# Performance work log

Measured on AMD Instinct MI355X. Metric: run time of the kernel, lower is better.

## Reference

```python
import jax, jax.numpy as jnp
import numpy as np

IN_F = 4096
OUT_F = 4096
SPARSITY = 0.98
N_TOKENS = 8192


def _structured_mask_and_weight(key):
    # Replicates _initialize_structured_sparsity: each output neuron i gets
    # connections_per_neuron contiguous (mod in_features) input columns
    # starting at (i * cpn) % in_features, with He-style init on those entries.
    num_conn = int((1.0 - SPARSITY) * IN_F * OUT_F)
    cpn = max(1, num_conn // OUT_F)  # connections per neuron (=81 here)
    rows = jnp.arange(OUT_F)[:, None]                      # [out, 1]
    cols = (rows * cpn + jnp.arange(cpn)[None, :]) % IN_F  # [out, cpn]
    mask = jnp.zeros((OUT_F, IN_F), jnp.float32).at[rows, cols].set(1.0)
    vals = jax.random.normal(key, (OUT_F, cpn), jnp.float32) * np.sqrt(2.0 / cpn)
    weight = jnp.zeros((OUT_F, IN_F), jnp.float32).at[rows, cols].set(vals)
    return mask, weight


def setup_inputs() -> dict:
    key = jax.random.key(0)
    k_w, k_b, k_x = jax.random.split(key, 3)
    mask, weight = _structured_mask_and_weight(k_w)
    gauge_field = jnp.ones((OUT_F, IN_F), jnp.float32)  # buffer initialized to ones
    bias = jax.random.normal(k_b, (OUT_F,), jnp.float32) * 0.01
    x = jax.random.normal(k_x, (N_TOKENS, IN_F), jnp.float32)
    return {"x": x, "weight": weight, "bias": bias,
            "mask": mask, "gauge_field": gauge_field}


def reference(x, weight, bias, mask, gauge_field):
    # effective_weight = weight * mask * gauge_field; F.linear(x, W, b) = x @ W.T + b
    effective_weight = weight * mask * gauge_field  # [out, in]
    return jnp.einsum('ni,oi->no', x, effective_weight) + bias
```

## Files before the change

### kernel.cpp

```cpp
#include <hip/hip_runtime.h>


typedef _Float16 h4 __attribute__((ext_vector_type(4)));
typedef _Float16 h8 __attribute__((ext_vector_type(8)));
typedef float f32x4 __attribute__((ext_vector_type(4)));

__global__ void __launch_bounds__(256) build_w4_kernel(
    const float* __restrict__ weight, const float* __restrict__ mask,
    const float* __restrict__ gauge, _Float16* __restrict__ w4) {
  int idx = blockIdx.x * 256 + threadIdx.x;
  int kk = idx % 96;
  int n  = (idx / 96) & 15;
  int m  = idx / 1536;
  int k  = m * 16 + n;
  float v = 0.f;
  if (kk >= n && kk < n + 81) {
    int o   = (2225 * k) & 4095;
    int col = (m * 16 + kk) & 4095;
    size_t off = (size_t)o * 4096 + col;
    v = weight[off] * mask[off] * gauge[off];
  }
  w4[idx] = (_Float16)v;
}

__global__ void __launch_bounds__(1024, 4) spmm_mfma_kernel(
    const float* __restrict__ x, const _Float16* __restrict__ w4,
    const float* __restrict__ bias, float* __restrict__ out) {
  __shared__ __align__(16) _Float16 xl[8 * 4104];
  __shared__ __align__(16) _Float16 ob[8 * 4104];

  const int tid = threadIdx.x;
  const size_t t0 = (size_t)blockIdx.x * 8;

  const float4* xg = (const float4*)(x + t0 * 4096);
#pragma unroll
  for (int i = 0; i < 8; ++i) {
    float4 v = xg[i * 1024 + tid];
    h4 hv = {(_Float16)v.x, (_Float16)v.y, (_Float16)v.z, (_Float16)v.w};
    *(h4*)&xl[i * 4104 + tid * 4] = hv;
  }
  __syncthreads();

  const int w = tid >> 6, lane = tid & 63;
  const int l15 = lane & 15, g = lane >> 4;
  const int tA = l15 & 7;
  const _Float16* xrow = xl + tA * 4104;
  const int aoff = 8 * g;
  const _Float16* bbase = w4 + (size_t)l15 * 96 + 8 * g;

  int m = w * 16;
  const _Float16* bp = bbase + (size_t)m * 1536;
  h8 b0 = *(const h8*)(bp);
  h8 b1 = *(const h8*)(bp + 32);
  h8 b2 = *(const h8*)(bp + 64);

#pragma unroll 2
  for (int i = 0; i < 16; ++i, ++m) {
    const int K16 = m << 4;
    const int o0 = (K16 + aoff) & 4095;
    const int o1 = (K16 + 32 + aoff) & 4095;
    const int o2 = (K16 + 64 + aoff) & 4095;
    h8 a0 = *(const h8*)(xrow + o0);
    h8 a1 = *(const h8*)(xrow + o1);
    h8 a2 = *(const h8*)(xrow + o2);
    h8 nb0, nb1, nb2;
    if (i < 15) {
      const _Float16* np = bbase + (size_t)(m + 1) * 1536;
      nb0 = *(const h8*)(np);
      nb1 = *(const h8*)(np + 32);
      nb2 = *(const h8*)(np + 64);
    } else { nb0 = b0; nb1 = b1; nb2 = b2; }
    f32x4 acc = {0.f, 0.f, 0.f, 0.f};
    acc = __builtin_amdgcn_mfma_f32_16x16x32_f16(a0, b0, acc, 0, 0, 0);
    acc = __builtin_amdgcn_mfma_f32_16x16x32_f16(a1, b1, acc, 0, 0, 0);
    acc = __builtin_amdgcn_mfma_f32_16x16x32_f16(a2, b2, acc, 0, 0, 0);
    if (lane < 32) {
      _Float16* op = ob + (g * 4) * 4104 + K16 + l15;
#pragma unroll
      for (int r = 0; r < 4; ++r) op[r * 4104] = (_Float16)acc[r];
    }
    b0 = nb0; b1 = nb1; b2 = nb2;
  }
  __syncthreads();

  float* og = out + t0 * 4096;
#pragma unroll
  for (int it = 0; it < 32; ++it) {
    int e = it * 1024 + tid;
    int tt = e >> 12, o = e & 4095;
    int k = (81 * o) & 4095;
    og[(size_t)tt * 4096 + o] = (float)ob[tt * 4104 + k] + bias[o];
  }
}

extern "C" void kernel_launch(void* const* d_in, const int* in_sizes, int n_in,
                              void* d_out, int out_size, void* d_ws, size_t ws_size,
                              hipStream_t stream) {
  const float* x      = (const float*)d_in[0];
  const float* weight = (const float*)d_in[1];
  const float* bias   = (const float*)d_in[2];
  const float* mask   = (const float*)d_in[3];
  const float* gauge  = (const float*)d_in[4];
  float* out = (float*)d_out;
  _Float16* w4 = (_Float16*)d_ws;

  build_w4_kernel<<<1536, 256, 0, stream>>>(weight, mask, gauge, w4);
  spmm_mfma_kernel<<<1024, 1024, 0, stream>>>(x, w4, bias, out);
}
```

Before: 358.0 us.

## Reuse x shared buffer for outputs in-place and halve block size

Drops the separate output shared buffer. Results are written back into the x tile in place, trailing the reads by 128 columns, with a barrier on every step and the first chunk held in registers until the end. The row is padded with a wrap-around copy so the masking on the x offsets can go, and blocks shrink to 512 threads, each wave handling 32 chunks. The epilogue writes float4 outputs and loads bias as float4. Halving LDS per block should allow more blocks per CU, at the cost of a __syncthreads in every loop iteration.

Measured after the change: 358.5 us. Within noise of the previous version (+0.2%).

```diff
diff --git a/kernel.cpp b/kernel.cpp
--- a/kernel.cpp
+++ b/kernel.cpp
@@ -4,6 +4,8 @@
 typedef _Float16 h4 __attribute__((ext_vector_type(4)));
 typedef _Float16 h8 __attribute__((ext_vector_type(8)));
 typedef float f32x4 __attribute__((ext_vector_type(4)));
+
+#define XS 4232
 
 __global__ void __launch_bounds__(256) build_w4_kernel(
     const float* __restrict__ weight, const float* __restrict__ mask,
@@ -23,73 +25,86 @@
   w4[idx] = (_Float16)v;
 }
 
-__global__ void __launch_bounds__(1024, 4) spmm_mfma_kernel(
+__global__ void __launch_bounds__(512, 4) spmm_mfma_kernel(
     const float* __restrict__ x, const _Float16* __restrict__ w4,
     const float* __restrict__ bias, float* __restrict__ out) {
-  __shared__ __align__(16) _Float16 xl[8 * 4104];
-  __shared__ __align__(16) _Float16 ob[8 * 4104];
+  __shared__ __align__(16) _Float16 xl[8 * XS];
 
   const int tid = threadIdx.x;
   const size_t t0 = (size_t)blockIdx.x * 8;
 
   const float4* xg = (const float4*)(x + t0 * 4096);
 #pragma unroll
-  for (int i = 0; i < 8; ++i) {
-    float4 v = xg[i * 1024 + tid];
+  for (int i = 0; i < 16; ++i) {
+    int idx = i * 512 + tid;
+    int row = idx >> 10, c4 = idx & 1023;
+    float4 v = xg[idx];
     h4 hv = {(_Float16)v.x, (_Float16)v.y, (_Float16)v.z, (_Float16)v.w};
-    *(h4*)&xl[i * 4104 + tid * 4] = hv;
+    *(h4*)&xl[row * XS + c4 * 4] = hv;
+    if (c4 < 24) *(h4*)&xl[row * XS + 4096 + c4 * 4] = hv;
   }
-  __syncthreads();
 
   const int w = tid >> 6, lane = tid & 63;
   const int l15 = lane & 15, g = lane >> 4;
   const int tA = l15 & 7;
-  const _Float16* xrow = xl + tA * 4104;
-  const int aoff = 8 * g;
+  const _Float16* xrow = xl + tA * XS;
   const _Float16* bbase = w4 + (size_t)l15 * 96 + 8 * g;
 
-  int m = w * 16;
-  const _Float16* bp = bbase + (size_t)m * 1536;
-  h8 b0 = *(const h8*)(bp);
-  h8 b1 = *(const h8*)(bp + 32);
-  h8 b2 = *(const h8*)(bp + 64);
+  const _Float16* bp0 = bbase + (size_t)w * 1536;
+  const _Float16* bp1 = bbase + (size_t)(8 + w) * 1536;
+  h8 b00 = *(const h8*)(bp0), b01 = *(const h8*)(bp0 + 32), b02 = *(const h8*)(bp0 + 64);
+  h8 b10 = *(const h8*)(bp1), b11 = *(const h8*)(bp1 + 32), b12 = *(const h8*)(bp1 + 64);
+
+  float h0, h1, h2, h3;
 
 #pragma unroll 2
-  for (int i = 0; i < 16; ++i, ++m) {
+  for (int s = 0; s < 32; ++s) {
+    const int m = 8 * s + w;
     const int K16 = m << 4;
-    const int o0 = (K16 + aoff) & 4095;
-    const int o1 = (K16 + 32 + aoff) & 4095;
-    const int o2 = (K16 + 64 + aoff) & 4095;
-    h8 a0 = *(const h8*)(xrow + o0);
-    h8 a1 = *(const h8*)(xrow + o1);
-    h8 a2 = *(const h8*)(xrow + o2);
-    h8 nb0, nb1, nb2;
-    if (i < 15) {
-      const _Float16* np = bbase + (size_t)(m + 1) * 1536;
-      nb0 = *(const h8*)(np);
-      nb1 = *(const h8*)(np + 32);
-      nb2 = *(const h8*)(np + 64);
-    } else { nb0 = b0; nb1 = b1; nb2 = b2; }
+    __syncthreads();
+    h8 a0 = *(const h8*)(xrow + K16 + 8 * g);
+    h8 a1 = *(const h8*)(xrow + K16 + 32 + 8 * g);
+    h8 a2 = *(const h8*)(xrow + K16 + 64 + 8 * g);
+    const _Float16* np = bbase + (size_t)(((m + 16) & 255)) * 1536;
+    h8 nb0 = *(const h8*)(np), nb1 = *(const h8*)(np + 32), nb2 = *(const h8*)(np + 64);
+
     f32x4 acc = {0.f, 0.f, 0.f, 0.f};
-    acc = __builtin_amdgcn_mfma_f32_16x16x32_f16(a0, b0, acc, 0, 0, 0);
-    acc = __builtin_amdgcn_mfma_f32_16x16x32_f16(a1, b1, acc, 0, 0, 0);
-    acc = __builtin_amdgcn_mfma_f32_16x16x32_f16(a2, b2, acc, 0, 0, 0);
-    if (lane < 32) {
-      _Float16* op = ob + (g * 4) * 4104 + K16 + l15;
+    acc = __builtin_amdgcn_mfma_f32_16x16x32_f16(a0, b00, acc, 0, 0, 0);
+    acc = __builtin_amdgcn_mfma_f32_16x16x32_f16(a1, b01, acc, 0, 0, 0);
+    acc = __builtin_amdgcn_mfma_f32_16x16x32_f16(a2, b02, acc, 0, 0, 0);
+
+    if (s == 0) {
+      h0 = acc[0]; h1 = acc[1]; h2 = acc[2]; h3 = acc[3];
+    } else if (lane < 32) {
+      _Float16* op = xl + K16 + l15 - 128 + (g * 4) * XS;
 #pragma unroll
-      for (int r = 0; r < 4; ++r) op[r * 4104] = (_Float16)acc[r];
+      for (int r = 0; r < 4; ++r) op[r * XS] = (_Float16)acc[r];
     }
-    b0 = nb0; b1 = nb1; b2 = nb2;
+    b00 = b10; b01 = b11; b02 = b12;
+    b10 = nb0; b11 = nb1; b12 = nb2;
+  }
+
+  __syncthreads();
+  if (lane < 32) {
+    _Float16* op = xl + 16 * w + l15 + 3968 + (g * 4) * XS;
+    op[0 * XS] = (_Float16)h0; op[1 * XS] = (_Float16)h1;
+    op[2 * XS] = (_Float16)h2; op[3 * XS] = (_Float16)h3;
   }
   __syncthreads();
 
   float* og = out + t0 * 4096;
 #pragma unroll
-  for (int it = 0; it < 32; ++it) {
-    int e = it * 1024 + tid;
+  for (int it = 0; it < 16; ++it) {
+    int e = (it * 512 + tid) * 4;
     int tt = e >> 12, o = e & 4095;
-    int k = (81 * o) & 4095;
-    og[(size_t)tt * 4096 + o] = (float)ob[tt * 4104 + k] + bias[o];
+    const _Float16* row = xl + tt * XS;
+    float4 bb = *(const float4*)(bias + o);
+    float4 r;
+    r.x = (float)row[(81 * o - 128) & 4095] + bb.x;
+    r.y = (float)row[(81 * o - 47) & 4095] + bb.y;
+    r.z = (float)row[(81 * o + 34) & 4095] + bb.z;
+    r.w = (float)row[(81 * o + 115) & 4095] + bb.w;
+    *(float4*)(og + e) = r;
   }
 }
 
@@ -105,5 +120,5 @@
   _Float16* w4 = (_Float16*)d_ws;
 
   build_w4_kernel<<<1536, 256, 0, stream>>>(weight, mask, gauge, w4);
-  spmm_mfma_kernel<<<1024, 1024, 0, stream>>>(x, w4, bias, out);
+  spmm_mfma_kernel<<<1024, 512, 0, stream>>>(x, w4, bias, out);
 }
```
